# Kernel tuning notes

Hardware: AMD Instinct MI355X
Metric: run time of the kernel (lower is better)

## Reference

```python
import jax, jax.numpy as jnp
import numpy as np
import math

E, H, FFN, NQ = 1024, 16, 4096, 8
B, T = 2, 2048
EPS = 1e-5

def layernorm(x, g, b):
    mu = jnp.mean(x, axis=-1, keepdims=True)
    var = jnp.mean(jnp.square(x - mu), axis=-1, keepdims=True)
    return (x - mu) * jax.lax.rsqrt(var + EPS) * g + b

def setup_inputs() -> dict:
    key = jax.random.key(0)
    ks = jax.random.split(key, 8)
    x = jax.random.normal(ks[0], (B, T, E), dtype=jnp.float32)
    mask = jnp.ones((B, T, T), dtype=bool)
    # constant quantum measurement output: PauliZ expectations of a fixed
    # RandomLayer circuit applied to |0..0> (independent of the input tokens)
    q_out = jax.random.uniform(ks[1], (NQ,), minval=-1.0, maxval=1.0, dtype=jnp.float32)
    s1 = 1.0 / math.sqrt(NQ)
    w1 = jax.random.uniform(ks[2], (NQ, FFN), minval=-s1, maxval=s1, dtype=jnp.float32)
    b1 = jnp.zeros((FFN,), dtype=jnp.float32)
    s2 = 1.0 / math.sqrt(FFN)
    w2 = jax.random.uniform(ks[3], (FFN, E), minval=-s2, maxval=s2, dtype=jnp.float32)
    b2 = jnp.zeros((E,), dtype=jnp.float32)
    g1 = jnp.ones((E,), dtype=jnp.float32); be1 = jnp.zeros((E,), dtype=jnp.float32)
    g2 = jnp.ones((E,), dtype=jnp.float32); be2 = jnp.zeros((E,), dtype=jnp.float32)
    return dict(x=x, mask=mask, q_out=q_out, w1=w1, b1=b1, w2=w2, b2=b2,
                g1=g1, be1=be1, g2=g2, be2=be2)

def reference(x, mask, q_out, w1, b1, w2, b2, g1, be1, g2, be2):
    b, t, e = x.shape
    d_k = e // H
    # q = k = v = head-split x (module has no QKV projections)
    q = x.reshape(b, t, H, d_k).transpose(0, 2, 1, 3)  # [B,H,T,d_k]
    scores = jnp.einsum('bhqd,bhkd->bhqk', q, q) / math.sqrt(d_k)
    scores = jnp.where(mask[:, None, :, :], scores, -1e9)
    attn = jax.nn.softmax(scores, axis=-1)
    out = jnp.einsum('bhqk,bhkd->bhqd', attn, q)
    attn_out = out.transpose(0, 2, 1, 3).reshape(b, t, e)
    x1 = layernorm(x + attn_out, g1, be1)
    # quantum FFN: constant measurement vector broadcast over all tokens
    h = jnp.broadcast_to(q_out, (b, t, NQ))
    h = jnp.dot(h, w1) + b1
    ffn_out = jnp.dot(jax.nn.relu(h), w2) + b2
    return layernorm(x1 + ffn_out, g2, be2)
```

## Files before the change

### kernel.cpp

```cpp
#include <hip/hip_runtime.h>

#define E_   1024
#define H_   16
#define DK_  64
#define FFN_ 4096
#define NQ_  8
#define B_   2
#define T_   2048
#define QBLK 128
#define KVBLK 64
#define NT_  (T_ / KVBLK)

#define NPART 256
#define ROWS_PER_PART (FFN_ / NPART)
#define CVT_BLOCKS (B_ * (T_ / 64) * H_)

typedef __attribute__((ext_vector_type(8))) __bf16 bf16x8;
typedef __attribute__((ext_vector_type(2))) __bf16 bf16x2;
typedef __attribute__((ext_vector_type(2))) float f32x2;
typedef __attribute__((ext_vector_type(4))) float f32x4;
typedef __attribute__((ext_vector_type(16))) float f32x16;

__device__ __forceinline__ __bf16 tobf(float f) { return (__bf16)f; }

__device__ __forceinline__ unsigned pk2(float a, float b) {
  f32x2 f; f[0] = a; f[1] = b;
  bf16x2 h = __builtin_convertvector(f, bf16x2);
  union { bf16x2 h; unsigned u; } u; u.h = h;
  return u.u;
}

__global__ __launch_bounds__(256)
void prep_kernel(const float* __restrict__ x, __bf16* __restrict__ xbf,
                 __bf16* __restrict__ xbfT,
                 const float* __restrict__ q_out, const float* __restrict__ w1,
                 const float* __restrict__ b1, const float* __restrict__ w2,
                 float* __restrict__ part) {
  const int tid = threadIdx.x;
  if (blockIdx.x < CVT_BLOCKS) {
    __shared__ __bf16 tile[64][66];
    const int bid = blockIdx.x;
    const int h  = bid & 15;
    const int tt = (bid >> 4) & 31;
    const int b  = bid >> 9;
    const float* src = x + ((size_t)(b * T_ + tt * 64)) * E_ + h * 64;
#pragma unroll
    for (int u = 0; u < 2; ++u) {
      const int idx = tid + 256 * u;
      const int r = idx >> 3;
      const int c = (idx & 7) * 8;
      float4 f0 = *reinterpret_cast<const float4*>(src + (size_t)r * E_ + c);
      float4 f1 = *reinterpret_cast<const float4*>(src + (size_t)r * E_ + c + 4);
      bf16x8 v;
      v[0] = tobf(f0.x); v[1] = tobf(f0.y); v[2] = tobf(f0.z); v[3] = tobf(f0.w);
      v[4] = tobf(f1.x); v[5] = tobf(f1.y); v[6] = tobf(f1.z); v[7] = tobf(f1.w);
      *reinterpret_cast<bf16x8*>(
          &xbf[((size_t)(b * T_ + tt * 64 + r)) * E_ + h * 64 + c]) = v;
#pragma unroll
      for (int j = 0; j < 8; ++j) tile[r][c + j] = v[j];
    }
    __syncthreads();
#pragma unroll
    for (int u = 0; u < 2; ++u) {
      const int idx = tid + 256 * u;
      const int d  = idx >> 3;
      const int tc = (idx & 7) * 8;
      bf16x8 v;
#pragma unroll
      for (int j = 0; j < 8; ++j) v[j] = tile[tc + j][d];
      *reinterpret_cast<bf16x8*>(
          &xbfT[((size_t)((b * H_ + h) * DK_ + d)) * T_ + tt * 64 + tc]) = v;
    }
  } else {
    __shared__ float hbuf[ROWS_PER_PART];
    const int p = blockIdx.x - CVT_BLOCKS;
    const int f0 = p * ROWS_PER_PART;
    if (tid < ROWS_PER_PART) {
      const int f = f0 + tid;
      float a = b1[f];
#pragma unroll
      for (int n = 0; n < NQ_; ++n) a += q_out[n] * w1[n * FFN_ + f];
      hbuf[tid] = fmaxf(a, 0.f);
    }
    __syncthreads();
    float4 acc = {0.f, 0.f, 0.f, 0.f};
#pragma unroll
    for (int j = 0; j < ROWS_PER_PART; ++j) {
      const float hf = hbuf[j];
      float4 w = reinterpret_cast<const float4*>(w2 + (size_t)(f0 + j) * E_)[tid];
      acc.x += hf * w.x; acc.y += hf * w.y; acc.z += hf * w.z; acc.w += hf * w.w;
    }
    reinterpret_cast<float4*>(part + (size_t)p * E_)[tid] = acc;
  }
}

__global__ __launch_bounds__(256)
void ffn_reduce_kernel(const float* __restrict__ part, const float* __restrict__ b2,
                       float* __restrict__ ffn_c) {
  const int e = blockIdx.x * 256 + threadIdx.x;
  float a = b2[e];
  for (int r = 0; r < NPART; ++r) a += part[(size_t)r * E_ + e];
  ffn_c[e] = a;
}

#define SM16(S, P)                                                             \
  do {                                                                         \
    _Pragma("unroll")                                                          \
    for (int m = 0; m < 4; ++m) {                                              \
      float e0 = __builtin_exp2f((S)[4 * m + 0]);                              \
      float e1 = __builtin_exp2f((S)[4 * m + 1]);                              \
      float e2 = __builtin_exp2f((S)[4 * m + 2]);                              \
      float e3 = __builtin_exp2f((S)[4 * m + 3]);                              \
      lg += (e0 + e1) + (e2 + e3);                                             \
      (P)[m][0] = pk2(e0, e1); (P)[m][1] = pk2(e2, e3);                        \
    }                                                                          \
  } while (0)

#define SWP(a, b) asm volatile("v_permlane32_swap_b32 %0, %1" : "+v"(a), "+v"(b))
#define SW4(P)                                                                 \
  do {                                                                         \
    SWP((P)[0][0], (P)[1][0]); SWP((P)[0][1], (P)[1][1]);                      \
    SWP((P)[2][0], (P)[3][0]); SWP((P)[2][1], (P)[3][1]);                      \
  } while (0)

#define PVQ(P, KSG)                                                            \
  do {                                                                         \
    union { unsigned u[4]; bf16x8 v; } pa;                                     \
    pa.u[0] = (P)[0][0]; pa.u[1] = (P)[0][1];                                  \
    pa.u[2] = (P)[1][0]; pa.u[3] = (P)[1][1];                                  \
    bf16x8 vb0 = *reinterpret_cast<const bf16x8*>(                             \
        Vtc + rowA + ((32 * (KSG) + 16 * hi) ^ rxA));                          \
    bf16x8 vb1 = *reinterpret_cast<const bf16x8*>(                             \
        Vtc + rowB + ((32 * (KSG) + 16 * hi) ^ rxB));                          \
    acc0 = __builtin_amdgcn_mfma_f32_32x32x16_bf16(pa.v, vb0, acc0, 0, 0, 0);  \
    acc1 = __builtin_amdgcn_mfma_f32_32x32x16_bf16(pa.v, vb1, acc1, 0, 0, 0);  \
    pa.u[0] = (P)[2][0]; pa.u[1] = (P)[2][1];                                  \
    pa.u[2] = (P)[3][0]; pa.u[3] = (P)[3][1];                                  \
    bf16x8 vc0 = *reinterpret_cast<const bf16x8*>(                             \
        Vtc + rowA + ((32 * ((KSG) + 1) + 16 * hi) ^ rxA));                    \
    bf16x8 vc1 = *reinterpret_cast<const bf16x8*>(                             \
        Vtc + rowB + ((32 * ((KSG) + 1) + 16 * hi) ^ rxB));                    \
    acc0 = __builtin_amdgcn_mfma_f32_32x32x16_bf16(pa.v, vc0, acc0, 0, 0, 0);  \
    acc1 = __builtin_amdgcn_mfma_f32_32x32x16_bf16(pa.v, vc1, acc1, 0, 0, 0);  \
  } while (0)

__global__ __launch_bounds__(256)
void attn_kernel(const __bf16* __restrict__ xbf, const __bf16* __restrict__ xbfT,
                 float* __restrict__ out) {
  __shared__ __bf16 Kt[2][KVBLK][DK_ + 8];
  __shared__ __bf16 VtF[2][DK_ * KVBLK];

  const int tid  = threadIdx.x;
  const int wave = tid >> 6;
  const int lane = tid & 63;
  const int l32  = lane & 31;
  const int hi   = lane >> 5;

  const int bh = blockIdx.y;
  const int b  = bh >> 4;
  const int h  = bh & 15;
  const int qbase = blockIdx.x * QBLK;
  const __bf16* xb = xbf + (size_t)b * T_ * E_ + h * DK_;

  bf16x8 qb[4];
  {
    const float sc = 0.125f * 1.44269504088896f;
    const __bf16* qrow = xb + (size_t)(qbase + wave * 32 + l32) * E_;
#pragma unroll
    for (int ks = 0; ks < 4; ++ks) {
      bf16x8 v = *reinterpret_cast<const bf16x8*>(qrow + 16 * ks + 8 * hi);
#pragma unroll
      for (int j = 0; j < 8; ++j) v[j] = tobf((float)v[j] * sc);
      qb[ks] = v;
    }
  }

  f32x16 acc0, acc1;
#pragma unroll
  for (int j = 0; j < 16; ++j) { acc0[j] = 0.f; acc1[j] = 0.f; }
  float lg = 0.f;

  const int rowA = l32 * 128;
  const int rxA  = ((l32 & 7) ^ ((l32 >> 3) & 7)) << 4;
  const int d2   = 32 + l32;
  const int rowB = d2 * 128;
  const int rxB  = ((d2 & 7) ^ ((d2 >> 3) & 7)) << 4;

  const int kp  = tid >> 3;
  const int ds0 = (tid & 7) * 8;
  const __bf16* kbase = xb + (size_t)(2 * kp) * E_ + ds0;
  const int dv = tid >> 3;
  const int kv = (tid & 7) * 8;
  const __bf16* vbase = xbfT + ((size_t)(bh * DK_ + dv)) * T_ + kv;
  const int srA = ((dv & 7) ^ ((dv >> 3) & 7)) << 4;
  const int dv2 = dv + 32;
  const int srB = ((dv2 & 7) ^ ((dv2 >> 3) & 7)) << 4;
  const int vbyteA = dv * 128 + ((kv * 2) ^ srA);
  const int vbyteB = dv2 * 128 + ((kv * 2) ^ srB);

  {
    uint4 k0 = *reinterpret_cast<const uint4*>(kbase);
    uint4 k1 = *reinterpret_cast<const uint4*>(kbase + E_);
    uint4 v0 = *reinterpret_cast<const uint4*>(vbase);
    uint4 v1 = *reinterpret_cast<const uint4*>(vbase + (size_t)32 * T_);
    *reinterpret_cast<uint4*>(&Kt[0][2 * kp][ds0])     = k0;
    *reinterpret_cast<uint4*>(&Kt[0][2 * kp + 1][ds0]) = k1;
    char* vb = reinterpret_cast<char*>(&VtF[0][0]);
    *reinterpret_cast<uint4*>(vb + vbyteA) = v0;
    *reinterpret_cast<uint4*>(vb + vbyteB) = v1;
  }
  __syncthreads();

  for (int t = 0; t < NT_; ++t) {
    const int cur = t & 1;
    const __bf16* Ktc = &Kt[cur][0][0];
    const char*   Vtc = reinterpret_cast<const char*>(&VtF[cur][0]);

    uint4 nk0, nk1, nv0, nv1;
    const bool have_next = (t + 1 < NT_);
    if (have_next) {
      const __bf16* nk = kbase + (size_t)(t + 1) * KVBLK * E_;
      const __bf16* nv = vbase + (size_t)(t + 1) * KVBLK;
      nk0 = *reinterpret_cast<const uint4*>(nk);
      nk1 = *reinterpret_cast<const uint4*>(nk + E_);
      nv0 = *reinterpret_cast<const uint4*>(nv);
      nv1 = *reinterpret_cast<const uint4*>(nv + (size_t)32 * T_);
    }

    f32x16 s0, s1;
#pragma unroll
    for (int j = 0; j < 16; ++j) { s0[j] = 0.f; s1[j] = 0.f; }
    __builtin_amdgcn_s_setprio(1);
#pragma unroll
    for (int ks = 0; ks < 4; ++ks) {
      bf16x8 ka0 = *reinterpret_cast<const bf16x8*>(
          Ktc + (size_t)l32 * (DK_ + 8) + 16 * ks + 8 * hi);
      bf16x8 ka1 = *reinterpret_cast<const bf16x8*>(
          Ktc + (size_t)(32 + l32) * (DK_ + 8) + 16 * ks + 8 * hi);
      s0 = __builtin_amdgcn_mfma_f32_32x32x16_bf16(ka0, qb[ks], s0, 0, 0, 0);
      s1 = __builtin_amdgcn_mfma_f32_32x32x16_bf16(ka1, qb[ks], s1, 0, 0, 0);
    }
    __builtin_amdgcn_s_setprio(0);

    unsigned dA_[4][2], dB_[4][2];
    SM16(s0, dA_);
    SM16(s1, dB_);
    SW4(dA_);
    SW4(dB_);

    __builtin_amdgcn_s_setprio(1);
    PVQ(dA_, 0);
    PVQ(dB_, 2);
    __builtin_amdgcn_s_setprio(0);

    if (have_next) {
      const int nxt = cur ^ 1;
      *reinterpret_cast<uint4*>(&Kt[nxt][2 * kp][ds0])     = nk0;
      *reinterpret_cast<uint4*>(&Kt[nxt][2 * kp + 1][ds0]) = nk1;
      char* vb = reinterpret_cast<char*>(&VtF[nxt][0]);
      *reinterpret_cast<uint4*>(vb + vbyteA) = nv0;
      *reinterpret_cast<uint4*>(vb + vbyteB) = nv1;
    }
    __syncthreads();
  }

  lg += __shfl_xor(lg, 32);
#pragma unroll
  for (int r = 0; r < 16; ++r) {
    const int qw = (r & 3) + 8 * (r >> 2) + 4 * hi;
    const float inv = 1.f / __shfl(lg, qw);
    const size_t q = (size_t)b * T_ + qbase + wave * 32 + qw;
    out[q * E_ + h * 64 + l32]      = acc0[r] * inv;
    out[q * E_ + h * 64 + 32 + l32] = acc1[r] * inv;
  }
}

__device__ __forceinline__ float block_sum(float v, float* redrow, int lane, int wave) {
#pragma unroll
  for (int off = 1; off < 64; off <<= 1) v += __shfl_xor(v, off);
  if (lane == 0) redrow[wave] = v;
  __syncthreads();
  return redrow[0] + redrow[1] + redrow[2] + redrow[3];
}

__global__ __launch_bounds__(256)
void ln_kernel(const float* __restrict__ x, const float* __restrict__ ffn_c,
               const float* __restrict__ g1, const float* __restrict__ be1,
               const float* __restrict__ g2, const float* __restrict__ be2,
               float* io) {
  __shared__ float red[4][4];
  const int row = blockIdx.x;
  const int tid = threadIdx.x;
  const int lane = tid & 63, wave = tid >> 6;
  const float* xr = x + (size_t)row * E_;
  float* ior = io + (size_t)row * E_;

  float4 xv = reinterpret_cast<const float4*>(xr)[tid];
  float4 av = reinterpret_cast<const float4*>(ior)[tid];
  float v[4] = {xv.x + av.x, xv.y + av.y, xv.z + av.z, xv.w + av.w};

  float mu1 = block_sum(v[0] + v[1] + v[2] + v[3], red[0], lane, wave) * (1.f / E_);
  float q1 = 0.f;
#pragma unroll
  for (int j = 0; j < 4; ++j) { float d = v[j] - mu1; q1 += d * d; }
  float var1 = block_sum(q1, red[1], lane, wave) * (1.f / E_);
  float rs1 = rsqrtf(var1 + 1e-5f);

  const int e0 = tid * 4;
  float y[4];
#pragma unroll
  for (int j = 0; j < 4; ++j)
    y[j] = (v[j] - mu1) * rs1 * g1[e0 + j] + be1[e0 + j] + ffn_c[e0 + j];

  float mu2 = block_sum(y[0] + y[1] + y[2] + y[3], red[2], lane, wave) * (1.f / E_);
  float q2 = 0.f;
#pragma unroll
  for (int j = 0; j < 4; ++j) { float d = y[j] - mu2; q2 += d * d; }
  float var2 = block_sum(q2, red[3], lane, wave) * (1.f / E_);
  float rs2 = rsqrtf(var2 + 1e-5f);

  float4 o;
  o.x = (y[0] - mu2) * rs2 * g2[e0 + 0] + be2[e0 + 0];
  o.y = (y[1] - mu2) * rs2 * g2[e0 + 1] + be2[e0 + 1];
  o.z = (y[2] - mu2) * rs2 * g2[e0 + 2] + be2[e0 + 2];
  o.w = (y[3] - mu2) * rs2 * g2[e0 + 3] + be2[e0 + 3];
  reinterpret_cast<float4*>(ior)[tid] = o;
}

extern "C" void kernel_launch(void* const* d_in, const int* in_sizes, int n_in,
                              void* d_out, int out_size, void* d_ws, size_t ws_size,
                              hipStream_t stream) {
  (void)in_sizes; (void)n_in; (void)out_size; (void)ws_size;
  const float* x     = (const float*)d_in[0];
  const float* q_out = (const float*)d_in[2];
  const float* w1    = (const float*)d_in[3];
  const float* b1    = (const float*)d_in[4];
  const float* w2    = (const float*)d_in[5];
  const float* b2    = (const float*)d_in[6];
  const float* g1    = (const float*)d_in[7];
  const float* be1   = (const float*)d_in[8];
  const float* g2    = (const float*)d_in[9];
  const float* be2   = (const float*)d_in[10];
  float* out   = (float*)d_out;

  float* ffn_c = (float*)d_ws;
  float* part  = ffn_c + E_;
  __bf16* xbf  = (__bf16*)(part + (size_t)NPART * E_);
  __bf16* xbfT = xbf + (size_t)B_ * T_ * E_;

  prep_kernel<<<CVT_BLOCKS + NPART, 256, 0, stream>>>(x, xbf, xbfT, q_out, w1,
                                                      b1, w2, part);
  ffn_reduce_kernel<<<E_ / 256, 256, 0, stream>>>(part, b2, ffn_c);
  dim3 ag(T_ / QBLK, B_ * H_);
  attn_kernel<<<ag, 256, 0, stream>>>(xbf, xbfT, out);
  ln_kernel<<<B_ * T_, 256, 0, stream>>>(x, ffn_c, g1, be1, g2, be2, out);
}
```

Baseline: 97.63 us.

## Split attention KV range across two blocks and merge partials in layernorm

Splits each query block's key/value sweep into two halves handled by separate workgroups, doubling the grid from 512 to 1024 blocks to better fill the GPU's compute units. Each half writes unnormalized accumulators and row sums, and the layernorm kernel combines the two partials and normalizes. Block indices are remapped so that consecutive blocks spread across XCDs. The cost is an extra full-size fp32 partial buffer written and read back. Merging without a max rescale is valid here only because the softmax never subtracts a running max.

```diff
diff --git a/kernel.cpp b/kernel.cpp
--- a/kernel.cpp
+++ b/kernel.cpp
@@ -9,7 +9,9 @@
 #define T_   2048
 #define QBLK 128
 #define KVBLK 64
-#define NT_  (T_ / KVBLK)
+#define KSPLIT 2
+#define NTS  (T_ / KVBLK / KSPLIT)
+#define NBLK ((T_ / QBLK) * B_ * H_ * KSPLIT)
 
 #define NPART 256
 #define ROWS_PER_PART (FFN_ / NPART)
@@ -146,7 +148,8 @@
 
 __global__ __launch_bounds__(256)
 void attn_kernel(const __bf16* __restrict__ xbf, const __bf16* __restrict__ xbfT,
-                 float* __restrict__ out) {
+                 float* __restrict__ On0, float* __restrict__ On1,
+                 float* __restrict__ lb0, float* __restrict__ lb1) {
   __shared__ __bf16 Kt[2][KVBLK][DK_ + 8];
   __shared__ __bf16 VtF[2][DK_ * KVBLK];
 
@@ -156,10 +159,15 @@
   const int l32  = lane & 31;
   const int hi   = lane >> 5;
 
-  const int bh = blockIdx.y;
+  const int lid  = ((blockIdx.x & 7) << 7) + (blockIdx.x >> 3);
+  const int bh   = lid >> 5;
+  const int rem  = lid & 31;
+  const int qblk = rem & 15;
+  const int ks   = rem >> 4;
   const int b  = bh >> 4;
   const int h  = bh & 15;
-  const int qbase = blockIdx.x * QBLK;
+  const int qbase = qblk * QBLK;
+  const int kofs  = ks * (T_ / KSPLIT);
   const __bf16* xb = xbf + (size_t)b * T_ * E_ + h * DK_;
 
   bf16x8 qb[4];
@@ -167,11 +175,11 @@
     const float sc = 0.125f * 1.44269504088896f;
     const __bf16* qrow = xb + (size_t)(qbase + wave * 32 + l32) * E_;
 #pragma unroll
-    for (int ks = 0; ks < 4; ++ks) {
-      bf16x8 v = *reinterpret_cast<const bf16x8*>(qrow + 16 * ks + 8 * hi);
+    for (int k2 = 0; k2 < 4; ++k2) {
+      bf16x8 v = *reinterpret_cast<const bf16x8*>(qrow + 16 * k2 + 8 * hi);
 #pragma unroll
       for (int j = 0; j < 8; ++j) v[j] = tobf((float)v[j] * sc);
-      qb[ks] = v;
+      qb[k2] = v;
     }
   }
 
@@ -188,10 +196,10 @@
 
   const int kp  = tid >> 3;
   const int ds0 = (tid & 7) * 8;
-  const __bf16* kbase = xb + (size_t)(2 * kp) * E_ + ds0;
+  const __bf16* kbase = xb + (size_t)(kofs + 2 * kp) * E_ + ds0;
   const int dv = tid >> 3;
   const int kv = (tid & 7) * 8;
-  const __bf16* vbase = xbfT + ((size_t)(bh * DK_ + dv)) * T_ + kv;
+  const __bf16* vbase = xbfT + ((size_t)(bh * DK_ + dv)) * T_ + kofs + kv;
   const int srA = ((dv & 7) ^ ((dv >> 3) & 7)) << 4;
   const int dv2 = dv + 32;
   const int srB = ((dv2 & 7) ^ ((dv2 >> 3) & 7)) << 4;
@@ -211,13 +219,13 @@
   }
   __syncthreads();
 
-  for (int t = 0; t < NT_; ++t) {
+  for (int t = 0; t < NTS; ++t) {
     const int cur = t & 1;
     const __bf16* Ktc = &Kt[cur][0][0];
     const char*   Vtc = reinterpret_cast<const char*>(&VtF[cur][0]);
 
     uint4 nk0, nk1, nv0, nv1;
-    const bool have_next = (t + 1 < NT_);
+    const bool have_next = (t + 1 < NTS);
     if (have_next) {
       const __bf16* nk = kbase + (size_t)(t + 1) * KVBLK * E_;
       const __bf16* nv = vbase + (size_t)(t + 1) * KVBLK;
@@ -232,13 +240,13 @@
     for (int j = 0; j < 16; ++j) { s0[j] = 0.f; s1[j] = 0.f; }
     __builtin_amdgcn_s_setprio(1);
 #pragma unroll
-    for (int ks = 0; ks < 4; ++ks) {
+    for (int k2 = 0; k2 < 4; ++k2) {
       bf16x8 ka0 = *reinterpret_cast<const bf16x8*>(
-          Ktc + (size_t)l32 * (DK_ + 8) + 16 * ks + 8 * hi);
+          Ktc + (size_t)l32 * (DK_ + 8) + 16 * k2 + 8 * hi);
       bf16x8 ka1 = *reinterpret_cast<const bf16x8*>(
-          Ktc + (size_t)(32 + l32) * (DK_ + 8) + 16 * ks + 8 * hi);
-      s0 = __builtin_amdgcn_mfma_f32_32x32x16_bf16(ka0, qb[ks], s0, 0, 0, 0);
-      s1 = __builtin_amdgcn_mfma_f32_32x32x16_bf16(ka1, qb[ks], s1, 0, 0, 0);
+          Ktc + (size_t)(32 + l32) * (DK_ + 8) + 16 * k2 + 8 * hi);
+      s0 = __builtin_amdgcn_mfma_f32_32x32x16_bf16(ka0, qb[k2], s0, 0, 0, 0);
+      s1 = __builtin_amdgcn_mfma_f32_32x32x16_bf16(ka1, qb[k2], s1, 0, 0, 0);
     }
     __builtin_amdgcn_s_setprio(0);
 
@@ -265,13 +273,16 @@
   }
 
   lg += __shfl_xor(lg, 32);
+  float* On = ks ? On1 : On0;
+  float* lb = ks ? lb1 : lb0;
+  if (hi == 0)
+    lb[(size_t)bh * T_ + qbase + wave * 32 + l32] = lg;
 #pragma unroll
   for (int r = 0; r < 16; ++r) {
     const int qw = (r & 3) + 8 * (r >> 2) + 4 * hi;
-    const float inv = 1.f / __shfl(lg, qw);
     const size_t q = (size_t)b * T_ + qbase + wave * 32 + qw;
-    out[q * E_ + h * 64 + l32]      = acc0[r] * inv;
-    out[q * E_ + h * 64 + 32 + l32] = acc1[r] * inv;
+    On[q * E_ + h * 64 + l32]      = acc0[r];
+    On[q * E_ + h * 64 + 32 + l32] = acc1[r];
   }
 }
 
@@ -284,7 +295,9 @@
 }
 
 __global__ __launch_bounds__(256)
-void ln_kernel(const float* __restrict__ x, const float* __restrict__ ffn_c,
+void ln_kernel(const float* __restrict__ x, const float* __restrict__ On1,
+               const float* __restrict__ lb0, const float* __restrict__ lb1,
+               const float* __restrict__ ffn_c,
                const float* __restrict__ g1, const float* __restrict__ be1,
                const float* __restrict__ g2, const float* __restrict__ be2,
                float* io) {
@@ -292,12 +305,21 @@
   const int row = blockIdx.x;
   const int tid = threadIdx.x;
   const int lane = tid & 63, wave = tid >> 6;
+  const int b = row >> 11;
+  const int q = row & (T_ - 1);
   const float* xr = x + (size_t)row * E_;
   float* ior = io + (size_t)row * E_;
 
+  const int e0 = tid * 4;
+  const int h = e0 >> 6;
+  const size_t lidx = ((size_t)(b * H_ + h)) * T_ + q;
+  const float invl = 1.f / (lb0[lidx] + lb1[lidx]);
+
   float4 xv = reinterpret_cast<const float4*>(xr)[tid];
-  float4 av = reinterpret_cast<const float4*>(ior)[tid];
-  float v[4] = {xv.x + av.x, xv.y + av.y, xv.z + av.z, xv.w + av.w};
+  float4 a1 = reinterpret_cast<const float4*>(ior)[tid];
+  float4 a2 = reinterpret_cast<const float4*>(On1 + (size_t)row * E_)[tid];
+  float v[4] = {xv.x + (a1.x + a2.x) * invl, xv.y + (a1.y + a2.y) * invl,
+                xv.z + (a1.z + a2.z) * invl, xv.w + (a1.w + a2.w) * invl};
 
   float mu1 = block_sum(v[0] + v[1] + v[2] + v[3], red[0], lane, wave) * (1.f / E_);
   float q1 = 0.f;
@@ -306,7 +328,6 @@
   float var1 = block_sum(q1, red[1], lane, wave) * (1.f / E_);
   float rs1 = rsqrtf(var1 + 1e-5f);
 
-  const int e0 = tid * 4;
   float y[4];
 #pragma unroll
   for (int j = 0; j < 4; ++j)
@@ -347,11 +368,14 @@
   float* part  = ffn_c + E_;
   __bf16* xbf  = (__bf16*)(part + (size_t)NPART * E_);
   __bf16* xbfT = xbf + (size_t)B_ * T_ * E_;
+  float* On1   = (float*)(xbfT + (size_t)B_ * T_ * E_);
+  float* lb0   = On1 + (size_t)B_ * T_ * E_;
+  float* lb1   = lb0 + (size_t)B_ * H_ * T_;
 
   prep_kernel<<<CVT_BLOCKS + NPART, 256, 0, stream>>>(x, xbf, xbfT, q_out, w1,
                                                       b1, w2, part);
   ffn_reduce_kernel<<<E_ / 256, 256, 0, stream>>>(part, b2, ffn_c);
-  dim3 ag(T_ / QBLK, B_ * H_);
-  attn_kernel<<<ag, 256, 0, stream>>>(xbf, xbfT, out);
-  ln_kernel<<<B_ * T_, 256, 0, stream>>>(x, ffn_c, g1, be1, g2, be2, out);
-}
+  attn_kernel<<<NBLK, 256, 0, stream>>>(xbf, xbfT, out, On1, lb0, lb1);
+  ln_kernel<<<B_ * T_, 256, 0, stream>>>(x, On1, lb0, lb1, ffn_c, g1, be1, g2,
+                                         be2, out);
+}
```

Measured after the change: 98.38 us. About the same (+0.8%).
